# Kernel optimization log

Hardware: AMD Instinct MI355X
Metric: run time of the kernel (lower is better)

## Reference

```python
import jax, jax.numpy as jnp
import numpy as np
import math

BINS = 256
SIGMA = 0.01
HMIN, HMAX = 0.0, 1.0


def soft_histogram(x, bins=BINS, vmin=HMIN, vmax=HMAX, sigma=SIGMA):
    # x: (B, C, H, W) -> histogram (B, C, bins)
    bin_centers = jnp.linspace(vmin, vmax, bins, dtype=x.dtype)  # (bins,)
    B, C = x.shape[0], x.shape[1]
    xf = x.reshape(B, C, -1, 1)                     # (B, C, N, 1)
    diff = xf - bin_centers.reshape(1, 1, 1, -1)    # (B, C, N, bins)
    norm = sigma * math.sqrt(2.0 * math.pi)
    weights = jnp.exp(-0.5 * (diff / sigma) ** 2) / norm
    hist = weights.sum(axis=2)                      # (B, C, bins)
    hist = hist / (hist.sum(axis=-1, keepdims=True) + 1e-10)
    return hist


def kl_divergence(p, q):
    eps = 1e-10
    p = p + eps
    q = q + eps
    return jnp.sum(p * jnp.log(p / q), axis=-1)


def setup_inputs() -> dict:
    key = jax.random.key(0)
    k1, k2 = jax.random.split(key)
    target = jax.random.uniform(k1, (8, 3, 128, 128), dtype=jnp.float32)
    prediction = jax.random.uniform(k2, (8, 3, 128, 128), dtype=jnp.float32)
    return {"target": target, "prediction": prediction}


def reference(target, prediction):
    target_hist = soft_histogram(target)
    pred_hist = soft_histogram(prediction)
    return kl_divergence(target_hist, pred_hist).mean()
```

## Files before the change

kernel.cpp:

```cpp
#include <hip/hip_runtime.h>
#include <math.h>

#define BINS   256
#define NPAIR  24
#define NPIX   16384
#define SPLIT  16
#define NBLK   (48 * SPLIT)

#define DELTA    0.003921568859f
#define NK2      -7213.475204f
#define A2K2     56.57627611f
#define B2K2     0.11093398f
#define RHO1     0.85745468f
#define RHO3     0.63042510f
#define RHO4     0.54056079f
#define INV_NORM 39.894228040143274f

typedef float v2f __attribute__((ext_vector_type(2)));

__global__ __launch_bounds__(256) void hist_kernel(
    const float* __restrict__ targ, const float* __restrict__ pred,
    float* __restrict__ g_part) {
  __shared__ float h[4][4][BINS];
  __shared__ float pxs[1024];

  const int t = threadIdx.x, lane = t & 63, wv = t >> 6;
  const int g = lane >> 4, lsub = lane & 15;
  const int pg = blockIdx.x >> 4;
  const int split = blockIdx.x & (SPLIT - 1);
  const int chan = (pg < NPAIR) ? pg : pg - NPAIR;
  const float* __restrict__ src = (pg < NPAIR) ? targ : pred;

  reinterpret_cast<float4*>(pxs)[t] =
      reinterpret_cast<const float4*>(src + chan * NPIX + split * 1024)[t];
  __syncthreads();

  const float c0 = (float)(16 * lsub) * DELTA;
  const v2f RHO13 = {RHO1, RHO3};
  const v2f RHO44 = {RHO4, RHO4};

  v2f acc[8];
  #pragma unroll
  for (int i = 0; i < 8; ++i) acc[i] = (v2f){0.f, 0.f};

  #pragma unroll 4
  for (int r = 0; r < 64; ++r) {
    const float x = pxs[wv * 256 + 4 * r + g];
    const float d = x - c0;
    const float w0 = __builtin_amdgcn_exp2f(NK2 * d * d);
    const float q0 = __builtin_amdgcn_exp2f(A2K2 * d - B2K2);

    v2f w; w.x = w0; w.y = w0 * q0;
    v2f m = (q0 * q0) * RHO13;
    acc[0] += w;
    #pragma unroll
    for (int i = 1; i < 8; ++i) {
      w *= m;
      m *= RHO44;
      acc[i] += w;
    }
  }

  #pragma unroll
  for (int i = 0; i < 8; i += 2)
    reinterpret_cast<float4*>(&h[wv][g][16 * lsub + 2 * i])[0] =
        make_float4(acc[i].x, acc[i].y, acc[i + 1].x, acc[i + 1].y);
  __syncthreads();

  float s = 0.f;
  #pragma unroll
  for (int w2 = 0; w2 < 4; ++w2)
    #pragma unroll
    for (int g2 = 0; g2 < 4; ++g2) s += h[w2][g2][t];
  g_part[blockIdx.x * BINS + t] = s;
}

__device__ __forceinline__ float wave_allsum(float v) {
  #pragma unroll
  for (int off = 32; off > 0; off >>= 1) v += __shfl_xor(v, off, 64);
  return v;
}
__device__ __forceinline__ float block_sum(float v, float* red, int lane, int wv) {
  v = wave_allsum(v);
  __syncthreads();
  if (lane == 0) red[wv] = v;
  __syncthreads();
  return red[0] + red[1] + red[2] + red[3];
}

__global__ __launch_bounds__(256) void klfused_kernel(
    const float* __restrict__ g_part, unsigned int* __restrict__ fl1,
    unsigned int* __restrict__ fl2, float* __restrict__ out) {
  const int t = threadIdx.x, lane = t & 63, wv = t >> 6;
  const int p = blockIdx.x;

  if (p < NPAIR) {
    __shared__ float red[4];
    float ht = 0.f, hq = 0.f;
    #pragma unroll
    for (int s = 0; s < SPLIT; ++s) {
      ht += g_part[(p * SPLIT + s) * BINS + t];
      hq += g_part[((NPAIR + p) * SPLIT + s) * BINS + t];
    }
    ht *= INV_NORM;
    hq *= INV_NORM;

    const float st = block_sum(ht, red, lane, wv);
    const float sq = block_sum(hq, red, lane, wv);
    const float P = ht / (st + 1e-10f) + 1e-10f;
    const float Q = hq / (sq + 1e-10f) + 1e-10f;
    const float kl = block_sum(P * __logf(P / Q), red, lane, wv);
    if (t == 0) {
      const unsigned int b = __float_as_uint(kl);
      __hip_atomic_store(&fl1[p], b, __ATOMIC_RELEASE, __HIP_MEMORY_SCOPE_AGENT);
      __hip_atomic_store(&fl2[p], ~b, __ATOMIC_RELEASE, __HIP_MEMORY_SCOPE_AGENT);
    }
  } else {
    if (t >= 64) return;
    float v = 0.f;
    if (lane < NPAIR) {
      unsigned int a, b;
      do {
        a = __hip_atomic_load(&fl1[lane], __ATOMIC_ACQUIRE, __HIP_MEMORY_SCOPE_AGENT);
        b = __hip_atomic_load(&fl2[lane], __ATOMIC_ACQUIRE, __HIP_MEMORY_SCOPE_AGENT);
      } while (b != ~a);
      v = __uint_as_float(a);
    }
    v = wave_allsum(v);
    if (lane == 0) out[0] = v * (1.0f / NPAIR);
  }
}

extern "C" void kernel_launch(void* const* d_in, const int* in_sizes, int n_in,
                              void* d_out, int out_size, void* d_ws, size_t ws_size,
                              hipStream_t stream) {
  const float* targ = (const float*)d_in[0];
  const float* pred = (const float*)d_in[1];
  float* g_part = (float*)d_ws;
  unsigned int* fl1 = (unsigned int*)(g_part + NBLK * BINS);
  unsigned int* fl2 = fl1 + NPAIR;
  float* out = (float*)d_out;

  hist_kernel<<<dim3(NBLK), dim3(256), 0, stream>>>(targ, pred, g_part);
  klfused_kernel<<<dim3(NPAIR + 1), dim3(256), 0, stream>>>(g_part, fl1, fl2, out);
}
```

Measured before the change: 21.93 us.

## Fuse histogram and KL kernels into one launch with flag-based inter-block sync

Merges the histogram kernel and the KL/reduction kernel into a single grid. Histogram blocks publish per-block completion flags, written as a magic value plus its complement, after a threadfence. KL blocks spin on the flags of their 32 producer blocks before reading the partials. This removes the second kernel launch and the gap between kernels. In exchange it relies on all blocks being co-resident to avoid deadlock, and flags left over from a previous call can be satisfied before the current data is written, which is a race.

```diff
diff --git a/kernel.cpp b/kernel.cpp
--- a/kernel.cpp
+++ b/kernel.cpp
@@ -15,64 +15,15 @@
 #define RHO3     0.63042510f
 #define RHO4     0.54056079f
 #define INV_NORM 39.894228040143274f
+#define HMAGIC   0xC0DE0000u
 
 typedef float v2f __attribute__((ext_vector_type(2)));
 
-__global__ __launch_bounds__(256) void hist_kernel(
-    const float* __restrict__ targ, const float* __restrict__ pred,
-    float* __restrict__ g_part) {
-  __shared__ float h[4][4][BINS];
-  __shared__ float pxs[1024];
-
-  const int t = threadIdx.x, lane = t & 63, wv = t >> 6;
-  const int g = lane >> 4, lsub = lane & 15;
-  const int pg = blockIdx.x >> 4;
-  const int split = blockIdx.x & (SPLIT - 1);
-  const int chan = (pg < NPAIR) ? pg : pg - NPAIR;
-  const float* __restrict__ src = (pg < NPAIR) ? targ : pred;
-
-  reinterpret_cast<float4*>(pxs)[t] =
-      reinterpret_cast<const float4*>(src + chan * NPIX + split * 1024)[t];
-  __syncthreads();
-
-  const float c0 = (float)(16 * lsub) * DELTA;
-  const v2f RHO13 = {RHO1, RHO3};
-  const v2f RHO44 = {RHO4, RHO4};
-
-  v2f acc[8];
-  #pragma unroll
-  for (int i = 0; i < 8; ++i) acc[i] = (v2f){0.f, 0.f};
-
-  #pragma unroll 4
-  for (int r = 0; r < 64; ++r) {
-    const float x = pxs[wv * 256 + 4 * r + g];
-    const float d = x - c0;
-    const float w0 = __builtin_amdgcn_exp2f(NK2 * d * d);
-    const float q0 = __builtin_amdgcn_exp2f(A2K2 * d - B2K2);
-
-    v2f w; w.x = w0; w.y = w0 * q0;
-    v2f m = (q0 * q0) * RHO13;
-    acc[0] += w;
-    #pragma unroll
-    for (int i = 1; i < 8; ++i) {
-      w *= m;
-      m *= RHO44;
-      acc[i] += w;
-    }
-  }
-
-  #pragma unroll
-  for (int i = 0; i < 8; i += 2)
-    reinterpret_cast<float4*>(&h[wv][g][16 * lsub + 2 * i])[0] =
-        make_float4(acc[i].x, acc[i].y, acc[i + 1].x, acc[i + 1].y);
-  __syncthreads();
-
-  float s = 0.f;
-  #pragma unroll
-  for (int w2 = 0; w2 < 4; ++w2)
-    #pragma unroll
-    for (int g2 = 0; g2 < 4; ++g2) s += h[w2][g2][t];
-  g_part[blockIdx.x * BINS + t] = s;
+__device__ __forceinline__ unsigned ld_acq(const unsigned* p) {
+  return __hip_atomic_load(p, __ATOMIC_ACQUIRE, __HIP_MEMORY_SCOPE_AGENT);
+}
+__device__ __forceinline__ void st_rel(unsigned* p, unsigned v) {
+  __hip_atomic_store(p, v, __ATOMIC_RELEASE, __HIP_MEMORY_SCOPE_AGENT);
 }
 
 __device__ __forceinline__ float wave_allsum(float v) {
@@ -88,14 +39,88 @@
   return red[0] + red[1] + red[2] + red[3];
 }
 
-__global__ __launch_bounds__(256) void klfused_kernel(
-    const float* __restrict__ g_part, unsigned int* __restrict__ fl1,
-    unsigned int* __restrict__ fl2, float* __restrict__ out) {
+__global__ __launch_bounds__(256) void fused_kernel(
+    const float* __restrict__ targ, const float* __restrict__ pred,
+    float* __restrict__ g_part, unsigned* __restrict__ hf1,
+    unsigned* __restrict__ hf2, unsigned* __restrict__ kf1,
+    unsigned* __restrict__ kf2, float* __restrict__ out) {
+  const int bid = blockIdx.x;
   const int t = threadIdx.x, lane = t & 63, wv = t >> 6;
-  const int p = blockIdx.x;
 
-  if (p < NPAIR) {
+  if (bid < NBLK) {
+    __shared__ float h[4][4][BINS];
+    __shared__ float pxs[1024];
+    const int g = lane >> 4, lsub = lane & 15;
+    const int pg = bid >> 4;
+    const int split = bid & (SPLIT - 1);
+    const int chan = (pg < NPAIR) ? pg : pg - NPAIR;
+    const float* __restrict__ src = (pg < NPAIR) ? targ : pred;
+
+    reinterpret_cast<float4*>(pxs)[t] =
+        reinterpret_cast<const float4*>(src + chan * NPIX + split * 1024)[t];
+    __syncthreads();
+
+    const float c0 = (float)(16 * lsub) * DELTA;
+    const v2f RHO13 = {RHO1, RHO3};
+    const v2f RHO44 = {RHO4, RHO4};
+
+    v2f acc[8];
+    #pragma unroll
+    for (int i = 0; i < 8; ++i) acc[i] = (v2f){0.f, 0.f};
+
+    #pragma unroll 4
+    for (int r = 0; r < 64; ++r) {
+      const float x = pxs[wv * 256 + 4 * r + g];
+      const float d = x - c0;
+      const float w0 = __builtin_amdgcn_exp2f(NK2 * d * d);
+      const float q0 = __builtin_amdgcn_exp2f(A2K2 * d - B2K2);
+
+      v2f w; w.x = w0; w.y = w0 * q0;
+      v2f m = (q0 * q0) * RHO13;
+      acc[0] += w;
+      #pragma unroll
+      for (int i = 1; i < 8; ++i) {
+        w *= m;
+        m *= RHO44;
+        acc[i] += w;
+      }
+    }
+
+    #pragma unroll
+    for (int i = 0; i < 8; i += 2)
+      reinterpret_cast<float4*>(&h[wv][g][16 * lsub + 2 * i])[0] =
+          make_float4(acc[i].x, acc[i].y, acc[i + 1].x, acc[i + 1].y);
+    __syncthreads();
+
+    float s = 0.f;
+    #pragma unroll
+    for (int w2 = 0; w2 < 4; ++w2)
+      #pragma unroll
+      for (int g2 = 0; g2 < 4; ++g2) s += h[w2][g2][t];
+    g_part[bid * BINS + t] = s;
+
+    __threadfence();
+    __syncthreads();
+    if (t == 0) {
+      st_rel(&hf1[bid], HMAGIC | (unsigned)bid);
+      st_rel(&hf2[bid], ~(HMAGIC | (unsigned)bid));
+    }
+
+  } else if (bid < NBLK + NPAIR) {
     __shared__ float red[4];
+    const int p = bid - NBLK;
+
+    if (wv == 0 && lane < 32) {
+      const int hb = (lane < 16) ? (p * SPLIT + lane)
+                                 : ((NPAIR + p) * SPLIT + (lane - 16));
+      unsigned a, b;
+      do {
+        a = ld_acq(&hf1[hb]);
+        b = ld_acq(&hf2[hb]);
+      } while (b != ~a);
+    }
+    __syncthreads();
+
     float ht = 0.f, hq = 0.f;
     #pragma unroll
     for (int s = 0; s < SPLIT; ++s) {
@@ -111,18 +136,19 @@
     const float Q = hq / (sq + 1e-10f) + 1e-10f;
     const float kl = block_sum(P * __logf(P / Q), red, lane, wv);
     if (t == 0) {
-      const unsigned int b = __float_as_uint(kl);
-      __hip_atomic_store(&fl1[p], b, __ATOMIC_RELEASE, __HIP_MEMORY_SCOPE_AGENT);
-      __hip_atomic_store(&fl2[p], ~b, __ATOMIC_RELEASE, __HIP_MEMORY_SCOPE_AGENT);
+      const unsigned b = __float_as_uint(kl);
+      st_rel(&kf1[p], b);
+      st_rel(&kf2[p], ~b);
     }
+
   } else {
     if (t >= 64) return;
     float v = 0.f;
     if (lane < NPAIR) {
-      unsigned int a, b;
+      unsigned a, b;
       do {
-        a = __hip_atomic_load(&fl1[lane], __ATOMIC_ACQUIRE, __HIP_MEMORY_SCOPE_AGENT);
-        b = __hip_atomic_load(&fl2[lane], __ATOMIC_ACQUIRE, __HIP_MEMORY_SCOPE_AGENT);
+        a = ld_acq(&kf1[lane]);
+        b = ld_acq(&kf2[lane]);
       } while (b != ~a);
       v = __uint_as_float(a);
     }
@@ -137,10 +163,12 @@
   const float* targ = (const float*)d_in[0];
   const float* pred = (const float*)d_in[1];
   float* g_part = (float*)d_ws;
-  unsigned int* fl1 = (unsigned int*)(g_part + NBLK * BINS);
-  unsigned int* fl2 = fl1 + NPAIR;
+  unsigned* hf1 = (unsigned*)(g_part + NBLK * BINS);
+  unsigned* hf2 = hf1 + NBLK;
+  unsigned* kf1 = hf2 + NBLK;
+  unsigned* kf2 = kf1 + NPAIR;
   float* out = (float*)d_out;
 
-  hist_kernel<<<dim3(NBLK), dim3(256), 0, stream>>>(targ, pred, g_part);
-  klfused_kernel<<<dim3(NPAIR + 1), dim3(256), 0, stream>>>(g_part, fl1, fl2, out);
+  fused_kernel<<<dim3(NBLK + NPAIR + 1), dim3(256), 0, stream>>>(
+      targ, pred, g_part, hf1, hf2, kf1, kf2, out);
 }
```

After: 74.62 us. +240.3%, slower.
